# Kernel tuning notes

Hardware: AMD Instinct MI355X
Metric: run time of the kernel (lower is better)

Reference implementation:

```python
import jax, jax.numpy as jnp
import numpy as np

MARGIN = 500.0


def setup_inputs() -> dict:
    key = jax.random.key(0)
    k1, k2 = jax.random.split(key)
    N, D = 32768, 3
    batched_labels = jax.random.randint(k1, (N,), 0, 100, dtype=jnp.int64 if jax.config.jax_enable_x64 else jnp.int32).astype(jnp.int32)
    batched_predicted_coords = jax.random.normal(k2, (N, D), dtype=jnp.float32)
    return {"batched_labels": batched_labels, "batched_predicted_coords": batched_predicted_coords}


def reference(batched_labels, batched_predicted_coords):
    # Faithful to the original: the Python loop overwrites `loss` each
    # iteration, so only the LAST anchor (i = N-1) contributes.
    anchor_lab = batched_labels[-1]
    anchor_pt = batched_predicted_coords[-1]  # [D]
    # labels: 0 if same label as anchor, 1 otherwise
    lab = jnp.where(batched_labels == anchor_lab, 0.0, 1.0)  # [N]
    diff = anchor_pt[None, :] - batched_predicted_coords  # [N, D]
    dist = jnp.sum(diff * diff, axis=1)  # squared euclidean distance, [N]
    loss = (1.0 - lab) * dist + lab * jnp.maximum(0.0, MARGIN - dist)
    return loss.sum()
```

## Files before the change

kernel.cpp:

```cpp
#include <hip/hip_runtime.h>

#define MARGIN 500.0f

__global__ __launch_bounds__(1024) void custom_loss_onepass(
        const int* __restrict__ labels,
        const float* __restrict__ coords,
        float* __restrict__ out, int N) {
    const int t = threadIdx.x;

    const int   anchor_lab = labels[N - 1];
    const float ax = coords[3 * (N - 1) + 0];
    const float ay = coords[3 * (N - 1) + 1];
    const float az = coords[3 * (N - 1) + 2];

    const float4* __restrict__ c4 = (const float4*)coords;
    const int4*   __restrict__ l4 = (const int4*)labels;

    const int ngroups = N >> 2;
    float v = 0.0f;
    for (int g = t; g < ngroups; g += 1024) {
        const float4 p0 = c4[3 * g + 0];
        const float4 p1 = c4[3 * g + 1];
        const float4 p2 = c4[3 * g + 2];
        const int4   lb = l4[g];
        {
            const float dx = ax - p0.x, dy = ay - p0.y, dz = az - p0.z;
            const float d = dx * dx + dy * dy + dz * dz;
            v += (lb.x == anchor_lab) ? d : fmaxf(0.0f, MARGIN - d);
        }
        {
            const float dx = ax - p0.w, dy = ay - p1.x, dz = az - p1.y;
            const float d = dx * dx + dy * dy + dz * dz;
            v += (lb.y == anchor_lab) ? d : fmaxf(0.0f, MARGIN - d);
        }
        {
            const float dx = ax - p1.z, dy = ay - p1.w, dz = az - p2.x;
            const float d = dx * dx + dy * dy + dz * dz;
            v += (lb.z == anchor_lab) ? d : fmaxf(0.0f, MARGIN - d);
        }
        {
            const float dx = ax - p2.y, dy = ay - p2.z, dz = az - p2.w;
            const float d = dx * dx + dy * dy + dz * dz;
            v += (lb.w == anchor_lab) ? d : fmaxf(0.0f, MARGIN - d);
        }
    }

    #pragma unroll
    for (int off = 32; off > 0; off >>= 1)
        v += __shfl_down(v, off, 64);

    __shared__ float smem[16];
    const int wave = t >> 6;
    const int lane = t & 63;
    if (lane == 0) smem[wave] = v;
    __syncthreads();

    if (t == 0) {
        float s = 0.0f;
        #pragma unroll
        for (int i = 0; i < 16; ++i) s += smem[i];
        out[0] = s;
    }
}

extern "C" void kernel_launch(void* const* d_in, const int* in_sizes, int n_in,
                              void* d_out, int out_size, void* d_ws, size_t ws_size,
                              hipStream_t stream) {
    const int*   labels = (const int*)d_in[0];
    const float* coords = (const float*)d_in[1];
    float*       out    = (float*)d_out;
    const int N = in_sizes[0];

    custom_loss_onepass<<<1, 1024, 0, stream>>>(labels, coords, out, N);
}
```

Measured before the change: 59.57 us.

## Split reduction across many blocks with a second-pass final reduce

Replaces the single 1024-thread block that loops over all points with a multi-block grid where each thread handles one group of four points and each block writes a partial sum to workspace. A second single-wave kernel then adds up the partials. This spreads the memory traffic over many compute units instead of one, at the cost of an extra kernel launch. The final kernel only reads the first 64 partials, so correctness depends on the grid having at most 64 blocks; with N=32768 the grid is 32.

```diff
diff --git a/kernel.cpp b/kernel.cpp
--- a/kernel.cpp
+++ b/kernel.cpp
@@ -2,12 +2,10 @@
 
 #define MARGIN 500.0f
 
-__global__ __launch_bounds__(1024) void custom_loss_onepass(
+__global__ __launch_bounds__(256) void loss_partial(
         const int* __restrict__ labels,
         const float* __restrict__ coords,
-        float* __restrict__ out, int N) {
-    const int t = threadIdx.x;
-
+        float* __restrict__ partial, int N) {
     const int   anchor_lab = labels[N - 1];
     const float ax = coords[3 * (N - 1) + 0];
     const float ay = coords[3 * (N - 1) + 1];
@@ -16,9 +14,9 @@
     const float4* __restrict__ c4 = (const float4*)coords;
     const int4*   __restrict__ l4 = (const int4*)labels;
 
-    const int ngroups = N >> 2;
+    const int g = blockIdx.x * blockDim.x + threadIdx.x;
     float v = 0.0f;
-    for (int g = t; g < ngroups; g += 1024) {
+    if (g < (N >> 2)) {
         const float4 p0 = c4[3 * g + 0];
         const float4 p1 = c4[3 * g + 1];
         const float4 p2 = c4[3 * g + 2];
@@ -49,18 +47,24 @@
     for (int off = 32; off > 0; off >>= 1)
         v += __shfl_down(v, off, 64);
 
-    __shared__ float smem[16];
-    const int wave = t >> 6;
-    const int lane = t & 63;
+    __shared__ float smem[4];
+    const int wave = threadIdx.x >> 6;
+    const int lane = threadIdx.x & 63;
     if (lane == 0) smem[wave] = v;
     __syncthreads();
 
-    if (t == 0) {
-        float s = 0.0f;
-        #pragma unroll
-        for (int i = 0; i < 16; ++i) s += smem[i];
-        out[0] = s;
-    }
+    if (threadIdx.x == 0)
+        partial[blockIdx.x] = smem[0] + smem[1] + smem[2] + smem[3];
+}
+
+__global__ __launch_bounds__(64) void loss_final(
+        const float* __restrict__ partial, float* __restrict__ out, int nparts) {
+    const int lane = threadIdx.x;
+    float v = (lane < nparts) ? partial[lane] : 0.0f;
+    #pragma unroll
+    for (int off = 32; off > 0; off >>= 1)
+        v += __shfl_down(v, off, 64);
+    if (lane == 0) out[0] = v;
 }
 
 extern "C" void kernel_launch(void* const* d_in, const int* in_sizes, int n_in,
@@ -69,7 +73,11 @@
     const int*   labels = (const int*)d_in[0];
     const float* coords = (const float*)d_in[1];
     float*       out    = (float*)d_out;
+    float*       partial = (float*)d_ws;
     const int N = in_sizes[0];
 
-    custom_loss_onepass<<<1, 1024, 0, stream>>>(labels, coords, out, N);
+    const int block = 256;
+    const int grid  = (N / 4 + block - 1) / block;
+    loss_partial<<<grid, block, 0, stream>>>(labels, coords, partial, N);
+    loss_final<<<1, 64, 0, stream>>>(partial, out, grid);
 }
```

Measured after the change: 57.18 us. 1.04x faster.
